# Kernel tuning notes

Measured on AMD Instinct MI355X. Metric: run time of the kernel, lower is better.

Reference implementation:

```python
import jax, jax.numpy as jnp
import numpy as np

N_NODES = 100000
N_EDGES = 1600000
NFEAT = 128
NHID = 128
NCLASS = 40
BN_EPS = 1e-5


def _glorot(key, shape):
    fan_in, fan_out = shape[1], shape[0]
    lim = (6.0 / (fan_in + fan_out)) ** 0.5
    return jax.random.uniform(key, shape, jnp.float32, -lim, lim)


def setup_inputs() -> dict:
    key = jax.random.key(0)
    ks = jax.random.split(key, 16)
    x = jax.random.normal(ks[0], (N_NODES, NFEAT), jnp.float32)
    src = jax.random.randint(ks[1], (N_EDGES,), 0, N_NODES, jnp.int64)
    dst = jax.random.randint(ks[2], (N_EDGES,), 0, N_NODES, jnp.int64)
    edge_index = jnp.stack([src, dst])  # [2, E]
    return {
        "x": x,
        "edge_index": edge_index,
        # conv1: nfeat -> nhid (lin_l with bias on aggregated msgs, lin_r no bias on root)
        "W1l": _glorot(ks[3], (NHID, NFEAT)), "b1": jnp.zeros((NHID,), jnp.float32),
        "W1r": _glorot(ks[4], (NHID, NFEAT)),
        # convx[0]: nhid -> nhid
        "Wxl": _glorot(ks[5], (NHID, NHID)), "bx": jnp.zeros((NHID,), jnp.float32),
        "Wxr": _glorot(ks[6], (NHID, NHID)),
        # conv2: nhid -> nclass
        "W2l": _glorot(ks[7], (NCLASS, NHID)), "b2": jnp.zeros((NCLASS,), jnp.float32),
        "W2r": _glorot(ks[8], (NCLASS, NHID)),
        # batch_norm3 (nhid) and batch_norm2 (nclass)
        "g3": jnp.ones((NHID,), jnp.float32), "be3": jnp.zeros((NHID,), jnp.float32),
        "g2": jnp.ones((NCLASS,), jnp.float32), "be2": jnp.zeros((NCLASS,), jnp.float32),
    }


def _sage_conv(x, src, dst, Wl, b, Wr):
    # mean aggregation of source features at destination nodes
    msg = x[src]                                                  # [E, F] gather
    agg = jax.ops.segment_sum(msg, dst, num_segments=N_NODES)    # [N, F] scatter-add
    cnt = jax.ops.segment_sum(jnp.ones((msg.shape[0],), x.dtype), dst, num_segments=N_NODES)
    mean = agg / jnp.maximum(cnt, 1.0)[:, None]                   # empty neighborhoods -> 0
    return mean @ Wl.T + b + x @ Wr.T


def _batch_norm(x, gamma, beta):
    mu = jnp.mean(x, axis=0)
    var = jnp.mean(jnp.square(x - mu), axis=0)  # biased var (training-mode BN)
    return (x - mu) * jax.lax.rsqrt(var + BN_EPS) * gamma + beta


def reference(x, edge_index, W1l, b1, W1r, Wxl, bx, Wxr, W2l, b2, W2r, g3, be3, g2, be2):
    src, dst = edge_index[0], edge_index[1]
    h = _sage_conv(x, src, dst, W1l, b1, W1r)      # conv1
    h = jax.nn.relu(h)
    # convx loop (nlayer - 2 == 1); dropout p=0 is identity
    h = _sage_conv(h, src, dst, Wxl, bx, Wxr)
    h = _batch_norm(h, g3, be3)                    # batch_norm3 (BN=True)
    h = jax.nn.relu(h)
    h = _sage_conv(h, src, dst, W2l, b2, W2r)      # conv2
    h = _batch_norm(h, g2, be2)                    # batch_norm2
    return h
```

## Files before the change

kernel.cpp:

```cpp
#include <hip/hip_runtime.h>
#include <hip/hip_bf16.h>

#define NN 100000
#define NE 1600000
#define NF 128
#define NC 40
#define BN_EPS 1e-5f

#define NB 256
#define NBU ((NN + 511) >> 9)
#define PT_TILE 4096
#define PT_GRID ((NE + PT_TILE - 1) / PT_TILE)

typedef __attribute__((ext_vector_type(8))) short short8;
typedef __attribute__((ext_vector_type(4))) float float4v;
typedef __attribute__((ext_vector_type(4))) int int4v;

__device__ __forceinline__ unsigned short f2b(float f) {
    __hip_bfloat16 h = __float2bfloat16(f);
    return *reinterpret_cast<unsigned short*>(&h);
}
__device__ __forceinline__ float b2f_hi(unsigned u) { return __uint_as_float(u & 0xffff0000u); }
__device__ __forceinline__ float b2f_lo(unsigned u) { return __uint_as_float(u << 16); }


__global__ __launch_bounds__(256) void bhist_kernel(const int* __restrict__ dst,
                                                    int* __restrict__ bhist) {
    __shared__ int lh[NB];
    int tid = threadIdx.x;
    lh[tid] = 0;
    __syncthreads();
    int base = blockIdx.x * PT_TILE;
    int cnt = min(PT_TILE, NE - base);
    const int4v* d4 = (const int4v*)(dst + base);
    int cnt4 = cnt >> 2;
    for (int i = tid; i < cnt4; i += 256) {
        int4v d = __builtin_nontemporal_load(d4 + i);
        atomicAdd(&lh[d[0] >> 9], 1);
        atomicAdd(&lh[d[1] >> 9], 1);
        atomicAdd(&lh[d[2] >> 9], 1);
        atomicAdd(&lh[d[3] >> 9], 1);
    }
    __syncthreads();
    if (lh[tid]) atomicAdd(&bhist[tid], lh[tid]);
}
// ... 107 lines not shown

__global__ __launch_bounds__(1024) void scan3_kernel(const int* __restrict__ deg,
                                                     const int* __restrict__ row_loc,
                                                     const int* __restrict__ blockoff,
                                                     int* __restrict__ row_ptr,
                                                     float* __restrict__ inv_cnt) {
    int i = blockIdx.x * 1024 + threadIdx.x;
    if (i < NN) {
        row_ptr[i] = blockoff[blockIdx.x] + row_loc[i];
        int d = deg[i];
        inv_cnt[i] = 1.0f / (float)(d > 0 ? d : 1);
    }
    if (i == 0) row_ptr[NN] = NE;
}

__global__ __launch_bounds__(256) void bucket_fill_kernel(const long long* __restrict__ stage,
                                                          const int* __restrict__ bbase,
                                                          const int* __restrict__ bcur,
                                                          const int* __restrict__ row_ptr,
                                                          int* __restrict__ cursor,
                                                          int* __restrict__ csr) {
    int b = blockIdx.x;
    int s = bbase[b], e = bcur[b];
    for (int i = s + threadIdx.x; i < e; i += 256) {
        long long p = __builtin_nontemporal_load(stage + i);
        int d = (int)(p & 0xffffffffLL);
        int sv = (int)(p >> 32);
        int pos = atomicAdd(&cursor[d], 1);
        csr[row_ptr[d] + pos] = sv;
    }
}


__global__ __launch_bounds__(256) void f2b4_kernel(const float* __restrict__ in,
                                                   unsigned short* __restrict__ out, int n4) {
    int i = blockIdx.x * 256 + threadIdx.x;
    if (i < n4) {
        float4 v = ((const float4*)in)[i];
        ushort4 o;
        o.x = f2b(v.x); o.y = f2b(v.y); o.z = f2b(v.z); o.w = f2b(v.w);
        ((ushort4*)out)[i] = o;
    }
}


__global__ __launch_bounds__(64) void pack_w_kernel(const float* __restrict__ Wl,
                                                    const float* __restrict__ Wr,
                                                    unsigned short* __restrict__ Bp) {
    int nt = blockIdx.x & 7;
    int kk = blockIdx.x >> 3;
    int lane = threadIdx.x;
    int n = nt * 16 + (lane & 15);
    int kb = kk * 32 + (lane >> 4) * 8;
    size_t base = ((size_t)(kk * 8 + nt) * 64 + lane) * 8;
#pragma unroll
    for (int j = 0; j < 8; ++j) {
        int k = kb + j;
        float v = (k < NF) ? Wl[(size_t)n * NF + k] : Wr[(size_t)n * NF + (k - NF)];
        Bp[base + j] = f2b(v);
    }
}

__global__ __launch_bounds__(64) void pack_w80_kernel(const float* __restrict__ Wl,
                                                      const float* __restrict__ Wr,
                                                      unsigned short* __restrict__ Bp) {
    int nt = blockIdx.x % 5;
    int kk = blockIdx.x / 5;
    int lane = threadIdx.x;
    int n = nt * 16 + (lane & 15);
    int kb = kk * 32 + (lane >> 4) * 8;
    size_t base = ((size_t)(kk * 5 + nt) * 64 + lane) * 8;
#pragma unroll
    for (int j = 0; j < 8; ++j) {
        int k = kb + j;
        float v = (n < NC) ? Wl[(size_t)n * NF + k] : Wr[(size_t)(n - NC) * NF + k];
        Bp[base + j] = f2b(v);
    }
}


__device__ __forceinline__ void acc8(float* a, uint4 u) {
    a[0] += b2f_lo(u.x); a[1] += b2f_hi(u.x);
    a[2] += b2f_lo(u.y); a[3] += b2f_hi(u.y);
    a[4] += b2f_lo(u.z); a[5] += b2f_hi(u.z);
    a[6] += b2f_lo(u.w); a[7] += b2f_hi(u.w);
}

__global__ __launch_bounds__(256) void agg_mean_bf16(const unsigned short* __restrict__ X,
                                                     const int* __restrict__ csr,
                                                     const int* __restrict__ row_ptr,
                                                     const float* __restrict__ inv_cnt,
                                                     unsigned short* __restrict__ out) {
    int tid = threadIdx.x;
    int lane = tid & 63;
    int wave = tid >> 6;
    int qw = lane >> 4;
    int sl = lane & 15;
    int n = blockIdx.x * 16 + wave * 4 + qw;
    if (n >= NN) return;
    int s = row_ptr[n], e = row_ptr[n + 1];
    int foff = sl * 8;

    float a[8];
#pragma unroll
    for (int j = 0; j < 8; ++j) a[j] = 0.f;

    int i = s;
    for (; i + 4 <= e; i += 4) {
        int s0 = csr[i], s1 = csr[i + 1], s2 = csr[i + 2], s3 = csr[i + 3];
        uint4 u0 = *(const uint4*)(X + (size_t)s0 * NF + foff);
        uint4 u1 = *(const uint4*)(X + (size_t)s1 * NF + foff);
        uint4 u2 = *(const uint4*)(X + (size_t)s2 * NF + foff);
        uint4 u3 = *(const uint4*)(X + (size_t)s3 * NF + foff);
        acc8(a, u0); acc8(a, u1); acc8(a, u2); acc8(a, u3);
    }
    for (; i < e; ++i) {
        uint4 u = *(const uint4*)(X + (size_t)csr[i] * NF + foff);
        acc8(a, u);
    }

    float ic = inv_cnt[n];
    uint4 o;
    o.x = (unsigned)f2b(a[0] * ic) | ((unsigned)f2b(a[1] * ic) << 16);
    o.y = (unsigned)f2b(a[2] * ic) | ((unsigned)f2b(a[3] * ic) << 16);
    o.z = (unsigned)f2b(a[4] * ic) | ((unsigned)f2b(a[5] * ic) << 16);
    o.w = (unsigned)f2b(a[6] * ic) | ((unsigned)f2b(a[7] * ic) << 16);
    *(uint4*)(out + (size_t)n * NF + foff) = o;
}


template <bool RELU>
__global__ __launch_bounds__(256, 5) void lin_mfma_kernel(const unsigned short* __restrict__ Ab,
                                                          const unsigned short* __restrict__ Xb,
                                                          const unsigned short* __restrict__ Bp,
                                                          const float* __restrict__ bias,
                                                          unsigned short* __restrict__ outb) {
    int tid = threadIdx.x;
    int wave = tid >> 6;
    int lane = tid & 63;
    int quad = lane >> 4;
    int row = blockIdx.x * 64 + wave * 16 + (lane & 15);
    int rowc = row < NN ? row : (NN - 1);
    const unsigned short* arow = Ab + (size_t)rowc * NF;
    const unsigned short* xrow = Xb + (size_t)rowc * NF;
    const short8* Bv = (const short8*)Bp;

    float4v acc[8];
#pragma unroll
    for (int nt = 0; nt < 8; ++nt) acc[nt] = (float4v){0.f, 0.f, 0.f, 0.f};

#pragma unroll
    for (int kk = 0; kk < 8; ++kk) {
        int kb = (kk & 3) * 32 + quad * 8;
        const unsigned short* asrc = (kk < 4) ? arow : xrow;
        short8 afrag = *(const short8*)(asrc + kb);
#pragma unroll
        for (int nt = 0; nt < 8; ++nt) {
            short8 bfrag = Bv[(kk * 8 + nt) * 64 + lane];
            acc[nt] = __builtin_amdgcn_mfma_f32_16x16x32_bf16(afrag, bfrag, acc[nt], 0, 0, 0);
        }
    }

    int orow = blockIdx.x * 64 + wave * 16 + quad * 4;
    int col = lane & 15;
#pragma unroll
    for (int nt = 0; nt < 8; ++nt) {
        int c = nt * 16 + col;
        float bv = bias[c];
#pragma unroll
        for (int r = 0; r < 4; ++r) {
            int rr = orow + r;
            if (rr < NN) {
                float v = acc[nt][r] + bv;
                if (RELU) v = fmaxf(v, 0.f);
                outb[(size_t)rr * NF + c] = f2b(v);
            }
        }
    }
}


__global__ __launch_bounds__(256, 5) void lin80_mfma_kernel(const unsigned short* __restrict__ Xb,
                                                            const unsigned short* __restrict__ Bp,
                                                            const float* __restrict__ b2,
                                                            unsigned short* __restrict__ t40,
                                                            float* __restrict__ z40) {
    int tid = threadIdx.x;
    int wave = tid >> 6;
    int lane = tid & 63;
    int quad = lane >> 4;
    int row = blockIdx.x * 64 + wave * 16 + (lane & 15);
    int rowc = row < NN ? row : (NN - 1);
    const unsigned short* xrow = Xb + (size_t)rowc * NF;
    const short8* Bv = (const short8*)Bp;

    float4v acc[5];
#pragma unroll
    for (int nt = 0; nt < 5; ++nt) acc[nt] = (float4v){0.f, 0.f, 0.f, 0.f};

#pragma unroll
    for (int kk = 0; kk < 4; ++kk) {
        int kb = kk * 32 + quad * 8;
        short8 afrag = *(const short8*)(xrow + kb);
#pragma unroll
        for (int nt = 0; nt < 5; ++nt) {
            short8 bfrag = Bv[(kk * 5 + nt) * 64 + lane];
            acc[nt] = __builtin_amdgcn_mfma_f32_16x16x32_bf16(afrag, bfrag, acc[nt], 0, 0, 0);
        }
    }

    int orow = blockIdx.x * 64 + wave * 16 + quad * 4;
    int col = lane & 15;
#pragma unroll
    for (int nt = 0; nt < 5; ++nt) {
        int c = nt * 16 + col;
#pragma unroll
        for (int r = 0; r < 4; ++r) {
            int rr = orow + r;
            if (rr < NN) {
                float v = acc[nt][r];
                if (c < NC) {
                    t40[(size_t)rr * NC + c] = f2b(v);
                } else {
                    z40[(size_t)rr * NC + (c - NC)] = v + b2[c - NC];
                }
            }
        }
    }
}


__global__ __launch_bounds__(256) void agg40_add_bf16(const unsigned short* __restrict__ T,
                                                      const float* __restrict__ Z,
                                                      const int* __restrict__ csr,
                                                      const int* __restrict__ row_ptr,
                                                      const float* __restrict__ inv_cnt,
                                                      float* __restrict__ out) {
    int tid = threadIdx.x;
    int lane = tid & 63;
    int wave = tid >> 6;
    if (lane >= 60) return;
    int sub = lane / 20;
    int sl = lane % 20;
    int n = blockIdx.x * 12 + wave * 3 + sub;
    if (n >= NN) return;
    int s = row_ptr[n], e = row_ptr[n + 1];
    float a0 = 0.f, a1 = 0.f;
    int i = s;
    for (; i + 4 <= e; i += 4) {
        int s0 = csr[i], s1 = csr[i + 1], s2 = csr[i + 2], s3 = csr[i + 3];
        unsigned u0 = *(const unsigned*)(T + (size_t)s0 * NC + sl * 2);
        unsigned u1 = *(const unsigned*)(T + (size_t)s1 * NC + sl * 2);
        unsigned u2 = *(const unsigned*)(T + (size_t)s2 * NC + sl * 2);
        unsigned u3 = *(const unsigned*)(T + (size_t)s3 * NC + sl * 2);
        a0 += b2f_lo(u0) + b2f_lo(u1) + b2f_lo(u2) + b2f_lo(u3);
        a1 += b2f_hi(u0) + b2f_hi(u1) + b2f_hi(u2) + b2f_hi(u3);
    }
    for (; i < e; ++i) {
        unsigned u = *(const unsigned*)(T + (size_t)csr[i] * NC + sl * 2);
        a0 += b2f_lo(u);
        a1 += b2f_hi(u);
    }
    float ic = inv_cnt[n];
    const float2 zv = *(const float2*)(Z + (size_t)n * NC + sl * 2);
    float2 o;
    o.x = a0 * ic + zv.x;
    o.y = a1 * ic + zv.y;
    *(float2*)(out + (size_t)n * NC + sl * 2) = o;
}

#define BN_GRID 640

template <int F>
__global__ __launch_bounds__(256) void bn_stats2_kernel(const float* __restrict__ X,
                                                        float* __restrict__ sums) {
    __shared__ float ls[2 * F];
    int tid = threadIdx.x;
    for (int i = tid; i < 2 * F; i += 256) ls[i] = 0.f;
    __syncthreads();

    const int total4 = NN * F / 4;
    const int stride = BN_GRID * 256;
    int i0 = blockIdx.x * 256 + tid;
    int c0 = (i0 * 4) % F;
    float s0 = 0.f, s1 = 0.f, s2 = 0.f, s3 = 0.f;
    float q0 = 0.f, q1 = 0.f, q2 = 0.f, q3 = 0.f;
    for (int i = i0; i < total4; i += stride) {
        float4 v = ((const float4*)X)[i];
        s0 += v.x; q0 += v.x * v.x;
        s1 += v.y; q1 += v.y * v.y;
        s2 += v.z; q2 += v.z * v.z;
        s3 += v.w; q3 += v.w * v.w;
    }
    atomicAdd(&ls[c0 + 0], s0); atomicAdd(&ls[F + c0 + 0], q0);
    atomicAdd(&ls[c0 + 1], s1); atomicAdd(&ls[F + c0 + 1], q1);
    atomicAdd(&ls[c0 + 2], s2); atomicAdd(&ls[F + c0 + 2], q2);
    atomicAdd(&ls[c0 + 3], s3); atomicAdd(&ls[F + c0 + 3], q3);
    __syncthreads();
    for (int i = tid; i < 2 * F; i += 256) atomicAdd(&sums[i], ls[i]);
}

__global__ __launch_bounds__(256) void bn_stats_b16_kernel(const unsigned short* __restrict__ H,
                                                           float* __restrict__ sums) {
    __shared__ float ls[2 * NF];
    int tid = threadIdx.x;
    for (int i = tid; i < 2 * NF; i += 256) ls[i] = 0.f;
    __syncthreads();

    const int total8 = NN * NF / 8;
    const int stride = BN_GRID * 256;
    int i0 = blockIdx.x * 256 + tid;
    int c0 = (i0 * 8) & (NF - 1);
    float s[8], q[8];
#pragma unroll
    for (int j = 0; j < 8; ++j) { s[j] = 0.f; q[j] = 0.f; }
    for (int i = i0; i < total8; i += stride) {
        uint4 u = ((const uint4*)H)[i];
        float v;
        v = b2f_lo(u.x); s[0] += v; q[0] += v * v;
        v = b2f_hi(u.x); s[1] += v; q[1] += v * v;
        v = b2f_lo(u.y); s[2] += v; q[2] += v * v;
        v = b2f_hi(u.y); s[3] += v; q[3] += v * v;
        v = b2f_lo(u.z); s[4] += v; q[4] += v * v;
        v = b2f_hi(u.z); s[5] += v; q[5] += v * v;
        v = b2f_lo(u.w); s[6] += v; q[6] += v * v;
        v = b2f_hi(u.w); s[7] += v; q[7] += v * v;
    }
#pragma unroll
    for (int j = 0; j < 8; ++j) {
        atomicAdd(&ls[c0 + j], s[j]);
        atomicAdd(&ls[NF + c0 + j], q[j]);
    }
    __syncthreads();
    for (int i = tid; i < 2 * NF; i += 256) atomicAdd(&sums[i], ls[i]);
}

__global__ __launch_bounds__(256) void bn3_apply_b16_kernel(unsigned* __restrict__ H,
                                                            const float* __restrict__ sums,
                                                            const float* __restrict__ g,
                                                            const float* __restrict__ be,
                                                            float invN) {
    int idx = blockIdx.x * 256 + threadIdx.x;
    if (idx >= NN * NF / 2) return;
    int t0 = (idx * 2) & (NF - 1);
    float mu0 = sums[t0] * invN, mu1 = sums[t0 + 1] * invN;
    float var0 = sums[NF + t0] * invN - mu0 * mu0;
    float var1 = sums[NF + t0 + 1] * invN - mu1 * mu1;
    float sc0 = rsqrtf(var0 + BN_EPS) * g[t0];
    float sc1 = rsqrtf(var1 + BN_EPS) * g[t0 + 1];
    unsigned u = H[idx];
    float v0 = fmaxf((b2f_lo(u) - mu0) * sc0 + be[t0], 0.f);
    float v1 = fmaxf((b2f_hi(u) - mu1) * sc1 + be[t0 + 1], 0.f);
    H[idx] = (unsigned)f2b(v0) | ((unsigned)f2b(v1) << 16);
}

template <bool RELU>
__global__ __launch_bounds__(256) void bn_apply_kernel(float* __restrict__ X,
                                                       const float* __restrict__ sums,
                                                       const float* __restrict__ g,
                                                       const float* __restrict__ be,
                                                       int F, float invN) {
    size_t idx = (size_t)blockIdx.x * blockDim.x + threadIdx.x;
    size_t total = (size_t)NN * F;
    if (idx >= total) return;
    int t = (int)(idx % F);
    float mu = sums[t] * invN;
    float var = sums[F + t] * invN - mu * mu;
    float scale = rsqrtf(var + BN_EPS) * g[t];
    float v = (X[idx] - mu) * scale + be[t];
    if (RELU) v = fmaxf(v, 0.f);
    X[idx] = v;
}


extern "C" void kernel_launch(void* const* d_in, const int* in_sizes, int n_in,
                              void* d_out, int out_size, void* d_ws, size_t ws_size,
                              hipStream_t stream) {
    const float* x   = (const float*)d_in[0];
    const int*   ei  = (const int*)d_in[1];
    const int*   srcv = ei;
    const int*   dstv = ei + NE;
    const float* W1l = (const float*)d_in[2];
    const float* b1  = (const float*)d_in[3];
    const float* W1r = (const float*)d_in[4];
    const float* Wxl = (const float*)d_in[5];
    const float* bx  = (const float*)d_in[6];
    const float* Wxr = (const float*)d_in[7];
    const float* W2l = (const float*)d_in[8];
    const float* b2  = (const float*)d_in[9];
    const float* W2r = (const float*)d_in[10];
    const float* g3  = (const float*)d_in[11];
    const float* be3 = (const float*)d_in[12];
    const float* g2  = (const float*)d_in[13];
    const float* be2 = (const float*)d_in[14];
    float* out = (float*)d_out;

    char* w = (char*)d_ws;
    unsigned short* xb   = (unsigned short*)w; w += (size_t)NN * NF * 2;
    unsigned short* h1b  = (unsigned short*)w; w += (size_t)NN * NF * 2;
    unsigned short* aggb = (unsigned short*)w; w += (size_t)NN * NF * 2;
    unsigned short* h2b  = (unsigned short*)w; w += (size_t)NN * NF * 2;
    int* csr     = (int*)w; w += (size_t)NE * 4;
    int* row_ptr = (int*)w; w += (size_t)(NN + 4) * 4;
    int* deg     = (int*)w; w += (size_t)NN * 4;
    int* cursor  = (int*)w; w += (size_t)NN * 4;
    int* row_loc = (int*)w; w += (size_t)NN * 4;
    int* blocksum = (int*)w; w += 128 * 4;
    float* inv_cnt = (float*)w; w += (size_t)NN * 4;
    float* bnbuf3  = (float*)w; w += 2 * NF * 4;
    float* bnbuf2  = (float*)w; w += 2 * NC * 4;
    unsigned short* Bp1 = (unsigned short*)w; w += (size_t)256 * NF * 2;
    unsigned short* Bpx = (unsigned short*)w; w += (size_t)256 * NF * 2;
    unsigned short* Bp2 = (unsigned short*)w; w += (size_t)128 * 80 * 2;
    int* bhist = (int*)w; w += NB * 4;
    int* bbase = (int*)w; w += NB * 4;
    int* bcurA = (int*)w; w += NB * 4;
    int2* stage = (int2*)h2b;
    unsigned short* t40 = xb;
    float* z40 = (float*)h1b;

    const int nscan = (NN + 1023) / 1024;

    hipMemsetAsync(deg, 0, (size_t)NN * 4, stream);
    hipMemsetAsync(cursor, 0, (size_t)NN * 4, stream);
    hipMemsetAsync(bhist, 0, NB * 4, stream);
    hipMemsetAsync(bnbuf3, 0, 2 * NF * 4, stream);
    hipMemsetAsync(bnbuf2, 0, 2 * NC * 4, stream);

    bhist_kernel<<<PT_GRID, 256, 0, stream>>>(dstv, bhist);
    bscan_kernel<<<1, 256, 0, stream>>>(bhist, bbase, bcurA);
    part_kernel<<<PT_GRID, 256, 0, stream>>>(srcv, dstv, bcurA, stage);
    bucket_deg_kernel<<<NBU, 256, 0, stream>>>((const long long*)stage, bbase, bcurA, deg);
    scan1_kernel<<<nscan, 1024, 0, stream>>>(deg, row_loc, blocksum);
    scan2_kernel<<<1, 128, 0, stream>>>(blocksum, nscan);
    scan3_kernel<<<nscan, 1024, 0, stream>>>(deg, row_loc, blocksum, row_ptr, inv_cnt);
    bucket_fill_kernel<<<NBU, 256, 0, stream>>>((const long long*)stage, bbase, bcurA,
                                                row_ptr, cursor, csr);

    f2b4_kernel<<<(NN * NF / 4 + 255) / 256, 256, 0, stream>>>(x, xb, NN * NF / 4);
    pack_w_kernel<<<64, 64, 0, stream>>>(W1l, W1r, Bp1);
    pack_w_kernel<<<64, 64, 0, stream>>>(Wxl, Wxr, Bpx);
    pack_w80_kernel<<<20, 64, 0, stream>>>(W2l, W2r, Bp2);

    const int nblk_lin = (NN + 63) / 64;
    const int nblk_agg = (NN + 15) / 16;

    agg_mean_bf16<<<nblk_agg, 256, 0, stream>>>(xb, csr, row_ptr, inv_cnt, aggb);
    lin_mfma_kernel<true><<<nblk_lin, 256, 0, stream>>>(aggb, xb, Bp1, b1, h1b);

    agg_mean_bf16<<<nblk_agg, 256, 0, stream>>>(h1b, csr, row_ptr, inv_cnt, aggb);
    lin_mfma_kernel<false><<<nblk_lin, 256, 0, stream>>>(aggb, h1b, Bpx, bx, h2b);

    bn_stats_b16_kernel<<<BN_GRID, 256, 0, stream>>>(h2b, bnbuf3);
    bn3_apply_b16_kernel<<<(NN * NF / 2 + 255) / 256, 256, 0, stream>>>((unsigned*)h2b, bnbuf3, g3, be3, 1.0f / NN);

    lin80_mfma_kernel<<<nblk_lin, 256, 0, stream>>>(h2b, Bp2, b2, t40, z40);
    agg40_add_bf16<<<(NN + 11) / 12, 256, 0, stream>>>(t40, z40, csr, row_ptr, inv_cnt, out);

    bn_stats2_kernel<NC><<<BN_GRID, 256, 0, stream>>>(out, bnbuf2);
    bn_apply_kernel<false><<<(NN * NC + 255) / 256, 256, 0, stream>>>(out, bnbuf2, g2, be2, NC, 1.0f / NN);
}
```

Baseline: 583.2 us.

## Fuse BN3 stats into linear epilogue, BN apply into lin80, degree-sort aggregation

Batch-norm statistics for the hidden layer are now accumulated in the MFMA linear kernel's epilogue, and the normalize+ReLU is applied on the fly when lin80 loads its A fragments. This removes a separate stats pass and an in-place apply pass over the 100k×128 bf16 tensor. Aggregation kernels now process nodes in degree-bucketed order via a counting-sort permutation and unroll the gather by 8, aiming to balance per-wave work and raise memory-level parallelism. The cost is three small extra preprocessing kernels plus shared/global atomics in the linear epilogue, and BN stats are now taken from fp32 values before bf16 rounding.

```diff
diff --git a/kernel.cpp b/kernel.cpp
--- a/kernel.cpp
+++ b/kernel.cpp
@@ -184,6 +184,66 @@
 }
 
 
+__global__ __launch_bounds__(256) void dhist_kernel(const int* __restrict__ deg,
+                                                    int* __restrict__ dh) {
+    __shared__ int lh[64];
+    int tid = threadIdx.x;
+    if (tid < 64) lh[tid] = 0;
+    __syncthreads();
+    int i0 = blockIdx.x * 1024 + tid;
+#pragma unroll
+    for (int j = 0; j < 4; ++j) {
+        int i = i0 + j * 256;
+        if (i < NN) atomicAdd(&lh[min(deg[i], 63)], 1);
+    }
+    __syncthreads();
+    if (tid < 64 && lh[tid]) atomicAdd(&dh[tid], lh[tid]);
+}
+
+__global__ __launch_bounds__(64) void dscan_kernel(const int* __restrict__ dh,
+                                                   int* __restrict__ dcur) {
+    int t = threadIdx.x;
+    int v = dh[t];
+    int x = v;
+    for (int off = 1; off < 64; off <<= 1) {
+        int u = __shfl_up(x, off);
+        if (t >= off) x += u;
+    }
+    dcur[t] = x - v;
+}
+
+__global__ __launch_bounds__(256) void dscatter_kernel(const int* __restrict__ deg,
+                                                       int* __restrict__ dcur,
+                                                       int* __restrict__ perm) {
+    __shared__ int lh[64], lb[64];
+    int tid = threadIdx.x;
+    if (tid < 64) lh[tid] = 0;
+    __syncthreads();
+    int i0 = blockIdx.x * 1024 + tid;
+#pragma unroll
+    for (int j = 0; j < 4; ++j) {
+        int i = i0 + j * 256;
+        if (i < NN) atomicAdd(&lh[min(deg[i], 63)], 1);
+    }
+    __syncthreads();
+    if (tid < 64) {
+        int c = lh[tid];
+        lb[tid] = (c > 0) ? atomicAdd(&dcur[tid], c) : 0;
+        lh[tid] = 0;
+    }
+    __syncthreads();
+#pragma unroll
+    for (int j = 0; j < 4; ++j) {
+        int i = i0 + j * 256;
+        if (i < NN) {
+            int b = min(deg[i], 63);
+            int p = atomicAdd(&lh[b], 1);
+            perm[lb[b] + p] = i;
+        }
+    }
+}
+
+
 __global__ __launch_bounds__(256) void f2b4_kernel(const float* __restrict__ in,
                                                    unsigned short* __restrict__ out, int n4) {
     int i = blockIdx.x * 256 + threadIdx.x;
@@ -242,32 +302,49 @@
                                                      const int* __restrict__ csr,
                                                      const int* __restrict__ row_ptr,
                                                      const float* __restrict__ inv_cnt,
+                                                     const int* __restrict__ perm,
                                                      unsigned short* __restrict__ out) {
     int tid = threadIdx.x;
     int lane = tid & 63;
     int wave = tid >> 6;
     int qw = lane >> 4;
     int sl = lane & 15;
-    int n = blockIdx.x * 16 + wave * 4 + qw;
-    if (n >= NN) return;
+    int g = blockIdx.x * 16 + wave * 4 + qw;
+    if (g >= NN) return;
+    int n = perm[g];
     int s = row_ptr[n], e = row_ptr[n + 1];
-    int foff = sl * 8;
+    const unsigned short* Xf = X + sl * 8;
 
     float a[8];
 #pragma unroll
     for (int j = 0; j < 8; ++j) a[j] = 0.f;
 
     int i = s;
-    for (; i + 4 <= e; i += 4) {
+    for (; i + 8 <= e; i += 8) {
         int s0 = csr[i], s1 = csr[i + 1], s2 = csr[i + 2], s3 = csr[i + 3];
-        uint4 u0 = *(const uint4*)(X + (size_t)s0 * NF + foff);
-        uint4 u1 = *(const uint4*)(X + (size_t)s1 * NF + foff);
-        uint4 u2 = *(const uint4*)(X + (size_t)s2 * NF + foff);
-        uint4 u3 = *(const uint4*)(X + (size_t)s3 * NF + foff);
+        int s4 = csr[i + 4], s5 = csr[i + 5], s6 = csr[i + 6], s7 = csr[i + 7];
+        uint4 u0 = *(const uint4*)(Xf + (size_t)s0 * NF);
+        uint4 u1 = *(const uint4*)(Xf + (size_t)s1 * NF);
+        uint4 u2 = *(const uint4*)(Xf + (size_t)s2 * NF);
+        uint4 u3 = *(const uint4*)(Xf + (size_t)s3 * NF);
+        uint4 u4 = *(const uint4*)(Xf + (size_t)s4 * NF);
+        uint4 u5 = *(const uint4*)(Xf + (size_t)s5 * NF);
+        uint4 u6 = *(const uint4*)(Xf + (size_t)s6 * NF);
+        uint4 u7 = *(const uint4*)(Xf + (size_t)s7 * NF);
         acc8(a, u0); acc8(a, u1); acc8(a, u2); acc8(a, u3);
+        acc8(a, u4); acc8(a, u5); acc8(a, u6); acc8(a, u7);
+    }
+    if (i + 4 <= e) {
+        int s0 = csr[i], s1 = csr[i + 1], s2 = csr[i + 2], s3 = csr[i + 3];
+        uint4 u0 = *(const uint4*)(Xf + (size_t)s0 * NF);
+        uint4 u1 = *(const uint4*)(Xf + (size_t)s1 * NF);
+        uint4 u2 = *(const uint4*)(Xf + (size_t)s2 * NF);
+        uint4 u3 = *(const uint4*)(Xf + (size_t)s3 * NF);
+        acc8(a, u0); acc8(a, u1); acc8(a, u2); acc8(a, u3);
+        i += 4;
     }
     for (; i < e; ++i) {
-        uint4 u = *(const uint4*)(X + (size_t)csr[i] * NF + foff);
+        uint4 u = *(const uint4*)(Xf + (size_t)csr[i] * NF);
         acc8(a, u);
     }
 
@@ -277,16 +354,18 @@
     o.y = (unsigned)f2b(a[2] * ic) | ((unsigned)f2b(a[3] * ic) << 16);
     o.z = (unsigned)f2b(a[4] * ic) | ((unsigned)f2b(a[5] * ic) << 16);
     o.w = (unsigned)f2b(a[6] * ic) | ((unsigned)f2b(a[7] * ic) << 16);
-    *(uint4*)(out + (size_t)n * NF + foff) = o;
-}
-
-
-template <bool RELU>
+    *(uint4*)(out + (size_t)n * NF + sl * 8) = o;
+}
+
+
+template <bool RELU, bool STATS>
 __global__ __launch_bounds__(256, 5) void lin_mfma_kernel(const unsigned short* __restrict__ Ab,
                                                           const unsigned short* __restrict__ Xb,
                                                           const unsigned short* __restrict__ Bp,
                                                           const float* __restrict__ bias,
-                                                          unsigned short* __restrict__ outb) {
+                                                          unsigned short* __restrict__ outb,
+                                                          float* __restrict__ sums) {
+    __shared__ float ls[256];
     int tid = threadIdx.x;
     int wave = tid >> 6;
     int lane = tid & 63;
@@ -297,6 +376,11 @@
     const unsigned short* xrow = Xb + (size_t)rowc * NF;
     const short8* Bv = (const short8*)Bp;
 
+    if (STATS) {
+        ls[tid] = 0.f;
+        __syncthreads();
+    }
+
     float4v acc[8];
 #pragma unroll
     for (int nt = 0; nt < 8; ++nt) acc[nt] = (float4v){0.f, 0.f, 0.f, 0.f};
@@ -319,22 +403,49 @@
     for (int nt = 0; nt < 8; ++nt) {
         int c = nt * 16 + col;
         float bv = bias[c];
+        float sv = 0.f, qv = 0.f;
 #pragma unroll
         for (int r = 0; r < 4; ++r) {
             int rr = orow + r;
             if (rr < NN) {
                 float v = acc[nt][r] + bv;
                 if (RELU) v = fmaxf(v, 0.f);
+                if (STATS) { sv += v; qv += v * v; }
                 outb[(size_t)rr * NF + c] = f2b(v);
             }
         }
-    }
+        if (STATS) {
+            atomicAdd(&ls[c], sv);
+            atomicAdd(&ls[128 + c], qv);
+        }
+    }
+    if (STATS) {
+        __syncthreads();
+        atomicAdd(&sums[tid], ls[tid]);
+    }
+}
+
+
+__global__ __launch_bounds__(128) void bn3_coef_kernel(const float* __restrict__ sums,
+                                                       const float* __restrict__ g,
+                                                       const float* __restrict__ be,
+                                                       float* __restrict__ sc,
+                                                       float* __restrict__ sh) {
+    int c = threadIdx.x;
+    float invN = 1.0f / (float)NN;
+    float mu = sums[c] * invN;
+    float var = sums[NF + c] * invN - mu * mu;
+    float s = rsqrtf(var + BN_EPS) * g[c];
+    sc[c] = s;
+    sh[c] = be[c] - mu * s;
 }
 
 
 __global__ __launch_bounds__(256, 5) void lin80_mfma_kernel(const unsigned short* __restrict__ Xb,
                                                             const unsigned short* __restrict__ Bp,
                                                             const float* __restrict__ b2,
+                                                            const float* __restrict__ bnsc,
+                                                            const float* __restrict__ bnsh,
                                                             unsigned short* __restrict__ t40,
                                                             float* __restrict__ z40) {
     int tid = threadIdx.x;
@@ -353,7 +464,20 @@
 #pragma unroll
     for (int kk = 0; kk < 4; ++kk) {
         int kb = kk * 32 + quad * 8;
-        short8 afrag = *(const short8*)(xrow + kb);
+        uint4 u = *(const uint4*)(xrow + kb);
+        float4 c0 = *(const float4*)(bnsc + kb);
+        float4 c1 = *(const float4*)(bnsc + kb + 4);
+        float4 h0 = *(const float4*)(bnsh + kb);
+        float4 h1 = *(const float4*)(bnsh + kb + 4);
+        short8 afrag;
+        afrag[0] = (short)f2b(fmaxf(b2f_lo(u.x) * c0.x + h0.x, 0.f));
+        afrag[1] = (short)f2b(fmaxf(b2f_hi(u.x) * c0.y + h0.y, 0.f));
+        afrag[2] = (short)f2b(fmaxf(b2f_lo(u.y) * c0.z + h0.z, 0.f));
+        afrag[3] = (short)f2b(fmaxf(b2f_hi(u.y) * c0.w + h0.w, 0.f));
+        afrag[4] = (short)f2b(fmaxf(b2f_lo(u.z) * c1.x + h1.x, 0.f));
+        afrag[5] = (short)f2b(fmaxf(b2f_hi(u.z) * c1.y + h1.y, 0.f));
+        afrag[6] = (short)f2b(fmaxf(b2f_lo(u.w) * c1.z + h1.z, 0.f));
+        afrag[7] = (short)f2b(fmaxf(b2f_hi(u.w) * c1.w + h1.w, 0.f));
 #pragma unroll
         for (int nt = 0; nt < 5; ++nt) {
             short8 bfrag = Bv[(kk * 5 + nt) * 64 + lane];
@@ -387,6 +511,7 @@
                                                       const int* __restrict__ csr,
                                                       const int* __restrict__ row_ptr,
                                                       const float* __restrict__ inv_cnt,
+                                                      const int* __restrict__ perm,
                                                       float* __restrict__ out) {
     int tid = threadIdx.x;
     int lane = tid & 63;
@@ -394,22 +519,41 @@
     if (lane >= 60) return;
     int sub = lane / 20;
     int sl = lane % 20;
-    int n = blockIdx.x * 12 + wave * 3 + sub;
-    if (n >= NN) return;
+    int g = blockIdx.x * 12 + wave * 3 + sub;
+    if (g >= NN) return;
+    int n = perm[g];
     int s = row_ptr[n], e = row_ptr[n + 1];
+    const unsigned short* Tf = T + sl * 2;
     float a0 = 0.f, a1 = 0.f;
     int i = s;
-    for (; i + 4 <= e; i += 4) {
+    for (; i + 8 <= e; i += 8) {
         int s0 = csr[i], s1 = csr[i + 1], s2 = csr[i + 2], s3 = csr[i + 3];
-        unsigned u0 = *(const unsigned*)(T + (size_t)s0 * NC + sl * 2);
-        unsigned u1 = *(const unsigned*)(T + (size_t)s1 * NC + sl * 2);
-        unsigned u2 = *(const unsigned*)(T + (size_t)s2 * NC + sl * 2);
-        unsigned u3 = *(const unsigned*)(T + (size_t)s3 * NC + sl * 2);
+        int s4 = csr[i + 4], s5 = csr[i + 5], s6 = csr[i + 6], s7 = csr[i + 7];
+        unsigned u0 = *(const unsigned*)(Tf + (size_t)s0 * NC);
+        unsigned u1 = *(const unsigned*)(Tf + (size_t)s1 * NC);
+        unsigned u2 = *(const unsigned*)(Tf + (size_t)s2 * NC);
+        unsigned u3 = *(const unsigned*)(Tf + (size_t)s3 * NC);
+        unsigned u4 = *(const unsigned*)(Tf + (size_t)s4 * NC);
+        unsigned u5 = *(const unsigned*)(Tf + (size_t)s5 * NC);
+        unsigned u6 = *(const unsigned*)(Tf + (size_t)s6 * NC);
+        unsigned u7 = *(const unsigned*)(Tf + (size_t)s7 * NC);
+        a0 += b2f_lo(u0) + b2f_lo(u1) + b2f_lo(u2) + b2f_lo(u3)
+            + b2f_lo(u4) + b2f_lo(u5) + b2f_lo(u6) + b2f_lo(u7);
+        a1 += b2f_hi(u0) + b2f_hi(u1) + b2f_hi(u2) + b2f_hi(u3)
+            + b2f_hi(u4) + b2f_hi(u5) + b2f_hi(u6) + b2f_hi(u7);
+    }
+    if (i + 4 <= e) {
+        int s0 = csr[i], s1 = csr[i + 1], s2 = csr[i + 2], s3 = csr[i + 3];
+        unsigned u0 = *(const unsigned*)(Tf + (size_t)s0 * NC);
+        unsigned u1 = *(const unsigned*)(Tf + (size_t)s1 * NC);
+        unsigned u2 = *(const unsigned*)(Tf + (size_t)s2 * NC);
+        unsigned u3 = *(const unsigned*)(Tf + (size_t)s3 * NC);
         a0 += b2f_lo(u0) + b2f_lo(u1) + b2f_lo(u2) + b2f_lo(u3);
         a1 += b2f_hi(u0) + b2f_hi(u1) + b2f_hi(u2) + b2f_hi(u3);
+        i += 4;
     }
     for (; i < e; ++i) {
-        unsigned u = *(const unsigned*)(T + (size_t)csr[i] * NC + sl * 2);
+        unsigned u = *(const unsigned*)(Tf + (size_t)csr[i] * NC);
         a0 += b2f_lo(u);
         a1 += b2f_hi(u);
     }
@@ -450,60 +594,6 @@
     atomicAdd(&ls[c0 + 3], s3); atomicAdd(&ls[F + c0 + 3], q3);
     __syncthreads();
     for (int i = tid; i < 2 * F; i += 256) atomicAdd(&sums[i], ls[i]);
-}
-
-__global__ __launch_bounds__(256) void bn_stats_b16_kernel(const unsigned short* __restrict__ H,
-                                                           float* __restrict__ sums) {
-    __shared__ float ls[2 * NF];
-    int tid = threadIdx.x;
-    for (int i = tid; i < 2 * NF; i += 256) ls[i] = 0.f;
-    __syncthreads();
-
-    const int total8 = NN * NF / 8;
-    const int stride = BN_GRID * 256;
-    int i0 = blockIdx.x * 256 + tid;
-    int c0 = (i0 * 8) & (NF - 1);
-    float s[8], q[8];
-#pragma unroll
-    for (int j = 0; j < 8; ++j) { s[j] = 0.f; q[j] = 0.f; }
-    for (int i = i0; i < total8; i += stride) {
-        uint4 u = ((const uint4*)H)[i];
-        float v;
-        v = b2f_lo(u.x); s[0] += v; q[0] += v * v;
-        v = b2f_hi(u.x); s[1] += v; q[1] += v * v;
-        v = b2f_lo(u.y); s[2] += v; q[2] += v * v;
-        v = b2f_hi(u.y); s[3] += v; q[3] += v * v;
-        v = b2f_lo(u.z); s[4] += v; q[4] += v * v;
-        v = b2f_hi(u.z); s[5] += v; q[5] += v * v;
-        v = b2f_lo(u.w); s[6] += v; q[6] += v * v;
-        v = b2f_hi(u.w); s[7] += v; q[7] += v * v;
-    }
-#pragma unroll
-    for (int j = 0; j < 8; ++j) {
-        atomicAdd(&ls[c0 + j], s[j]);
-        atomicAdd(&ls[NF + c0 + j], q[j]);
-    }
-    __syncthreads();
-    for (int i = tid; i < 2 * NF; i += 256) atomicAdd(&sums[i], ls[i]);
-}
-
-__global__ __launch_bounds__(256) void bn3_apply_b16_kernel(unsigned* __restrict__ H,
-                                                            const float* __restrict__ sums,
-                                                            const float* __restrict__ g,
-                                                            const float* __restrict__ be,
-                                                            float invN) {
-    int idx = blockIdx.x * 256 + threadIdx.x;
-    if (idx >= NN * NF / 2) return;
-    int t0 = (idx * 2) & (NF - 1);
-    float mu0 = sums[t0] * invN, mu1 = sums[t0 + 1] * invN;
-    float var0 = sums[NF + t0] * invN - mu0 * mu0;
-    float var1 = sums[NF + t0 + 1] * invN - mu1 * mu1;
-    float sc0 = rsqrtf(var0 + BN_EPS) * g[t0];
-    float sc1 = rsqrtf(var1 + BN_EPS) * g[t0 + 1];
-    unsigned u = H[idx];
-    float v0 = fmaxf((b2f_lo(u) - mu0) * sc0 + be[t0], 0.f);
-    float v1 = fmaxf((b2f_hi(u) - mu1) * sc1 + be[t0 + 1], 0.f);
-    H[idx] = (unsigned)f2b(v0) | ((unsigned)f2b(v1) << 16);
 }
 
 template <bool RELU>
@@ -561,12 +651,17 @@
     float* inv_cnt = (float*)w; w += (size_t)NN * 4;
     float* bnbuf3  = (float*)w; w += 2 * NF * 4;
     float* bnbuf2  = (float*)w; w += 2 * NC * 4;
+    float* bnsc    = (float*)w; w += NF * 4;
+    float* bnsh    = (float*)w; w += NF * 4;
     unsigned short* Bp1 = (unsigned short*)w; w += (size_t)256 * NF * 2;
     unsigned short* Bpx = (unsigned short*)w; w += (size_t)256 * NF * 2;
     unsigned short* Bp2 = (unsigned short*)w; w += (size_t)128 * 80 * 2;
     int* bhist = (int*)w; w += NB * 4;
     int* bbase = (int*)w; w += NB * 4;
     int* bcurA = (int*)w; w += NB * 4;
+    int* dh    = (int*)w; w += 64 * 4;
+    int* dcur  = (int*)w; w += 64 * 4;
+    int* perm  = (int*)w; w += (size_t)NN * 4;
     int2* stage = (int2*)h2b;
     unsigned short* t40 = xb;
     float* z40 = (float*)h1b;
@@ -576,6 +671,7 @@
     hipMemsetAsync(deg, 0, (size_t)NN * 4, stream);
     hipMemsetAsync(cursor, 0, (size_t)NN * 4, stream);
     hipMemsetAsync(bhist, 0, NB * 4, stream);
+    hipMemsetAsync(dh, 0, 64 * 4, stream);
     hipMemsetAsync(bnbuf3, 0, 2 * NF * 4, stream);
     hipMemsetAsync(bnbuf2, 0, 2 * NC * 4, stream);
 
@@ -583,6 +679,9 @@
     bscan_kernel<<<1, 256, 0, stream>>>(bhist, bbase, bcurA);
     part_kernel<<<PT_GRID, 256, 0, stream>>>(srcv, dstv, bcurA, stage);
     bucket_deg_kernel<<<NBU, 256, 0, stream>>>((const long long*)stage, bbase, bcurA, deg);
+    dhist_kernel<<<nscan, 256, 0, stream>>>(deg, dh);
+    dscan_kernel<<<1, 64, 0, stream>>>(dh, dcur);
+    dscatter_kernel<<<nscan, 256, 0, stream>>>(deg, dcur, perm);
     scan1_kernel<<<nscan, 1024, 0, stream>>>(deg, row_loc, blocksum);
     scan2_kernel<<<1, 128, 0, stream>>>(blocksum, nscan);
     scan3_kernel<<<nscan, 1024, 0, stream>>>(deg, row_loc, blocksum, row_ptr, inv_cnt);
@@ -597,17 +696,16 @@
     const int nblk_lin = (NN + 63) / 64;
     const int nblk_agg = (NN + 15) / 16;
 
-    agg_mean_bf16<<<nblk_agg, 256, 0, stream>>>(xb, csr, row_ptr, inv_cnt, aggb);
-    lin_mfma_kernel<true><<<nblk_lin, 256, 0, stream>>>(aggb, xb, Bp1, b1, h1b);
-
-    agg_mean_bf16<<<nblk_agg, 256, 0, stream>>>(h1b, csr, row_ptr, inv_cnt, aggb);
-    lin_mfma_kernel<false><<<nblk_lin, 256, 0, stream>>>(aggb, h1b, Bpx, bx, h2b);
-
-    bn_stats_b16_kernel<<<BN_GRID, 256, 0, stream>>>(h2b, bnbuf3);
-    bn3_apply_b16_kernel<<<(NN * NF / 2 + 255) / 256, 256, 0, stream>>>((unsigned*)h2b, bnbuf3, g3, be3, 1.0f / NN);
-
-    lin80_mfma_kernel<<<nblk_lin, 256, 0, stream>>>(h2b, Bp2, b2, t40, z40);
-    agg40_add_bf16<<<(NN + 11) / 12, 256, 0, stream>>>(t40, z40, csr, row_ptr, inv_cnt, out);
+    agg_mean_bf16<<<nblk_agg, 256, 0, stream>>>(xb, csr, row_ptr, inv_cnt, perm, aggb);
+    lin_mfma_kernel<true, false><<<nblk_lin, 256, 0, stream>>>(aggb, xb, Bp1, b1, h1b, nullptr);
+
+    agg_mean_bf16<<<nblk_agg, 256, 0, stream>>>(h1b, csr, row_ptr, inv_cnt, perm, aggb);
+    lin_mfma_kernel<false, true><<<nblk_lin, 256, 0, stream>>>(aggb, h1b, Bpx, bx, h2b, bnbuf3);
+
+    bn3_coef_kernel<<<1, 128, 0, stream>>>(bnbuf3, g3, be3, bnsc, bnsh);
+
+    lin80_mfma_kernel<<<nblk_lin, 256, 0, stream>>>(h2b, Bp2, b2, bnsc, bnsh, t40, z40);
+    agg40_add_bf16<<<(NN + 11) / 12, 256, 0, stream>>>(t40, z40, csr, row_ptr, inv_cnt, perm, out);
 
     bn_stats2_kernel<NC><<<BN_GRID, 256, 0, stream>>>(out, bnbuf2);
     bn_apply_kernel<false><<<(NN * NC + 255) / 256, 256, 0, stream>>>(out, bnbuf2, g2, be2, NC, 1.0f / NN);
```

Measured after the change: 601.2 us. +3.1%, slower.

## Fuse BN3 stats into convx GEMM and BN3 apply into conv2 GEMM

Applied to the files above, without the earlier changes.

The linear kernels become persistent grid-stride loops that keep the packed weight fragments in registers and swap MFMA operands, so each wave owns column slices and writes vectorised outputs. The convx GEMM accumulates per-column sum and sum-of-squares into banked atomics, and a tiny kernel turns them into scale/shift. The conv2 GEMM then applies BN and ReLU on the fly when loading its input, which removes the separate stats pass and the read-modify-write apply pass over h2. In exchange, BN statistics are now computed from fp32 values before bf16 rounding, and more registers are held per thread.

```diff
diff --git a/kernel.cpp b/kernel.cpp
--- a/kernel.cpp
+++ b/kernel.cpp
@@ -11,6 +11,10 @@
 #define NBU ((NN + 511) >> 9)
 #define PT_TILE 4096
 #define PT_GRID ((NE + PT_TILE - 1) / PT_TILE)
+#define SBANK 32
+#define NTILES (NN / 16)
+#define LIN_GRID 1250
+#define LIN80_GRID 512
 
 typedef __attribute__((ext_vector_type(8))) short short8;
 typedef __attribute__((ext_vector_type(4))) float float4v;
@@ -281,101 +285,217 @@
 }
 
 
-template <bool RELU>
-__global__ __launch_bounds__(256, 5) void lin_mfma_kernel(const unsigned short* __restrict__ Ab,
-                                                          const unsigned short* __restrict__ Xb,
-                                                          const unsigned short* __restrict__ Bp,
-                                                          const float* __restrict__ bias,
-                                                          unsigned short* __restrict__ outb) {
+template <bool RELU, bool STATS>
+__device__ __forceinline__ void lin_body(const unsigned short* __restrict__ Ab,
+                                         const unsigned short* __restrict__ Xb,
+                                         const unsigned short* __restrict__ Bp,
+                                         const float* __restrict__ bias,
+                                         unsigned short* __restrict__ outb,
+                                         float* __restrict__ sums,
+                                         float* ls) {
     int tid = threadIdx.x;
     int wave = tid >> 6;
     int lane = tid & 63;
     int quad = lane >> 4;
-    int row = blockIdx.x * 64 + wave * 16 + (lane & 15);
-    int rowc = row < NN ? row : (NN - 1);
-    const unsigned short* arow = Ab + (size_t)rowc * NF;
-    const unsigned short* xrow = Xb + (size_t)rowc * NF;
+    int sl = lane & 15;
     const short8* Bv = (const short8*)Bp;
 
-    float4v acc[8];
-#pragma unroll
-    for (int nt = 0; nt < 8; ++nt) acc[nt] = (float4v){0.f, 0.f, 0.f, 0.f};
-
-#pragma unroll
-    for (int kk = 0; kk < 8; ++kk) {
-        int kb = (kk & 3) * 32 + quad * 8;
-        const unsigned short* asrc = (kk < 4) ? arow : xrow;
-        short8 afrag = *(const short8*)(asrc + kb);
-#pragma unroll
-        for (int nt = 0; nt < 8; ++nt) {
-            short8 bfrag = Bv[(kk * 8 + nt) * 64 + lane];
-            acc[nt] = __builtin_amdgcn_mfma_f32_16x16x32_bf16(afrag, bfrag, acc[nt], 0, 0, 0);
+    if (STATS) {
+        ls[tid] = 0.f;
+        __syncthreads();
+    }
+
+    short8 bfr[8][2];
+#pragma unroll
+    for (int kk = 0; kk < 8; ++kk)
+#pragma unroll
+        for (int j = 0; j < 2; ++j)
+            bfr[kk][j] = Bv[(kk * 8 + 2 * wave + j) * 64 + lane];
+
+    float4 bias4[2];
+#pragma unroll
+    for (int j = 0; j < 2; ++j)
+        bias4[j] = *(const float4*)(bias + (2 * wave + j) * 16 + quad * 4);
+
+    float sts[2][4], stq[2][4];
+    if (STATS) {
+#pragma unroll
+        for (int j = 0; j < 2; ++j)
+#pragma unroll
+            for (int r = 0; r < 4; ++r) { sts[j][r] = 0.f; stq[j][r] = 0.f; }
+    }
+
+    for (int t = blockIdx.x; t < NTILES; t += LIN_GRID) {
+        int rr = t * 16 + sl;
+        const unsigned short* arow = Ab + (size_t)rr * NF;
+        const unsigned short* xrow = Xb + (size_t)rr * NF;
+
+        short8 xf[8];
+#pragma unroll
+        for (int kk = 0; kk < 8; ++kk) {
+            int kb = (kk & 3) * 32 + quad * 8;
+            const unsigned short* asrc = (kk < 4) ? arow : xrow;
+            xf[kk] = *(const short8*)(asrc + kb);
         }
-    }
-
-    int orow = blockIdx.x * 64 + wave * 16 + quad * 4;
-    int col = lane & 15;
-#pragma unroll
-    for (int nt = 0; nt < 8; ++nt) {
-        int c = nt * 16 + col;
-        float bv = bias[c];
-#pragma unroll
-        for (int r = 0; r < 4; ++r) {
-            int rr = orow + r;
-            if (rr < NN) {
-                float v = acc[nt][r] + bv;
-                if (RELU) v = fmaxf(v, 0.f);
-                outb[(size_t)rr * NF + c] = f2b(v);
+
+        float4v acc[2];
+#pragma unroll
+        for (int j = 0; j < 2; ++j) acc[j] = (float4v){0.f, 0.f, 0.f, 0.f};
+
+#pragma unroll
+        for (int kk = 0; kk < 8; ++kk)
+#pragma unroll
+            for (int j = 0; j < 2; ++j)
+                acc[j] = __builtin_amdgcn_mfma_f32_16x16x32_bf16(bfr[kk][j], xf[kk], acc[j], 0, 0, 0);
+
+#pragma unroll
+        for (int j = 0; j < 2; ++j) {
+            int c0 = (2 * wave + j) * 16 + quad * 4;
+            float v0 = acc[j][0] + bias4[j].x;
+            float v1 = acc[j][1] + bias4[j].y;
+            float v2 = acc[j][2] + bias4[j].z;
+            float v3 = acc[j][3] + bias4[j].w;
+            if (RELU) {
+                v0 = fmaxf(v0, 0.f); v1 = fmaxf(v1, 0.f);
+                v2 = fmaxf(v2, 0.f); v3 = fmaxf(v3, 0.f);
+            }
+            if (STATS) {
+                sts[j][0] += v0; stq[j][0] += v0 * v0;
+                sts[j][1] += v1; stq[j][1] += v1 * v1;
+                sts[j][2] += v2; stq[j][2] += v2 * v2;
+                sts[j][3] += v3; stq[j][3] += v3 * v3;
+            }
+            ushort4 o;
+            o.x = f2b(v0); o.y = f2b(v1); o.z = f2b(v2); o.w = f2b(v3);
+            *(ushort4*)(outb + (size_t)rr * NF + c0) = o;
+        }
+    }
+
+    if (STATS) {
+#pragma unroll
+        for (int j = 0; j < 2; ++j) {
+            int c0 = (2 * wave + j) * 16 + quad * 4;
+#pragma unroll
+            for (int r = 0; r < 4; ++r) {
+                atomicAdd(&ls[c0 + r], sts[j][r]);
+                atomicAdd(&ls[128 + c0 + r], stq[j][r]);
             }
         }
-    }
-}
-
-
-__global__ __launch_bounds__(256, 5) void lin80_mfma_kernel(const unsigned short* __restrict__ Xb,
+        __syncthreads();
+        atomicAdd(&sums[(blockIdx.x & (SBANK - 1)) * 256 + tid], ls[tid]);
+    }
+}
+
+__global__ __launch_bounds__(256, 3) void lin_conv1_kernel(const unsigned short* __restrict__ Ab,
+                                                           const unsigned short* __restrict__ Xb,
+                                                           const unsigned short* __restrict__ Bp,
+                                                           const float* __restrict__ bias,
+                                                           unsigned short* __restrict__ outb) {
+    lin_body<true, false>(Ab, Xb, Bp, bias, outb, nullptr, nullptr);
+}
+
+__global__ __launch_bounds__(256, 3) void lin_convx_kernel(const unsigned short* __restrict__ Ab,
+                                                           const unsigned short* __restrict__ Xb,
+                                                           const unsigned short* __restrict__ Bp,
+                                                           const float* __restrict__ bias,
+                                                           unsigned short* __restrict__ outb,
+                                                           float* __restrict__ sums) {
+    __shared__ float ls[256];
+    lin_body<false, true>(Ab, Xb, Bp, bias, outb, sums, ls);
+}
+
+
+__global__ __launch_bounds__(128) void bn3_coef_kernel(const float* __restrict__ sums,
+                                                       const float* __restrict__ g,
+                                                       const float* __restrict__ be,
+                                                       float* __restrict__ sc,
+                                                       float* __restrict__ sh) {
+    int c = threadIdx.x;
+    float sv = 0.f, qv = 0.f;
+    for (int b = 0; b < SBANK; ++b) {
+        sv += sums[b * 256 + c];
+        qv += sums[b * 256 + 128 + c];
+    }
+    float invN = 1.0f / (float)NN;
+    float mu = sv * invN;
+    float var = qv * invN - mu * mu;
+    float s = rsqrtf(var + BN_EPS) * g[c];
+    sc[c] = s;
+    sh[c] = be[c] - mu * s;
+}
+
+
+__global__ __launch_bounds__(256, 2) void lin80_mfma_kernel(const unsigned short* __restrict__ Xb,
                                                             const unsigned short* __restrict__ Bp,
                                                             const float* __restrict__ b2,
+                                                            const float* __restrict__ bnsc,
+                                                            const float* __restrict__ bnsh,
                                                             unsigned short* __restrict__ t40,
                                                             float* __restrict__ z40) {
     int tid = threadIdx.x;
     int wave = tid >> 6;
     int lane = tid & 63;
     int quad = lane >> 4;
-    int row = blockIdx.x * 64 + wave * 16 + (lane & 15);
-    int rowc = row < NN ? row : (NN - 1);
-    const unsigned short* xrow = Xb + (size_t)rowc * NF;
+    int sl = lane & 15;
     const short8* Bv = (const short8*)Bp;
 
-    float4v acc[5];
-#pragma unroll
-    for (int nt = 0; nt < 5; ++nt) acc[nt] = (float4v){0.f, 0.f, 0.f, 0.f};
-
+    short8 bfr[4][5];
+#pragma unroll
+    for (int kk = 0; kk < 4; ++kk)
+#pragma unroll
+        for (int nt = 0; nt < 5; ++nt)
+            bfr[kk][nt] = Bv[(kk * 5 + nt) * 64 + lane];
+
+    float4 sc0[4], sc1[4], sh0[4], sh1[4];
 #pragma unroll
     for (int kk = 0; kk < 4; ++kk) {
         int kb = kk * 32 + quad * 8;
-        short8 afrag = *(const short8*)(xrow + kb);
+        sc0[kk] = *(const float4*)(bnsc + kb);
+        sc1[kk] = *(const float4*)(bnsc + kb + 4);
+        sh0[kk] = *(const float4*)(bnsh + kb);
+        sh1[kk] = *(const float4*)(bnsh + kb + 4);
+    }
+
+    int gw = blockIdx.x * 4 + wave;
+    for (int t = gw; t < NTILES; t += LIN80_GRID * 4) {
+        int rr = t * 16 + sl;
+        const unsigned short* xrow = Xb + (size_t)rr * NF;
+
+        float4v acc[5];
+#pragma unroll
+        for (int nt = 0; nt < 5; ++nt) acc[nt] = (float4v){0.f, 0.f, 0.f, 0.f};
+
+#pragma unroll
+        for (int kk = 0; kk < 4; ++kk) {
+            uint4 u = *(const uint4*)(xrow + kk * 32 + quad * 8);
+            short8 xf;
+            xf[0] = (short)f2b(fmaxf(b2f_lo(u.x) * sc0[kk].x + sh0[kk].x, 0.f));
+            xf[1] = (short)f2b(fmaxf(b2f_hi(u.x) * sc0[kk].y + sh0[kk].y, 0.f));
+            xf[2] = (short)f2b(fmaxf(b2f_lo(u.y) * sc0[kk].z + sh0[kk].z, 0.f));
+            xf[3] = (short)f2b(fmaxf(b2f_hi(u.y) * sc0[kk].w + sh0[kk].w, 0.f));
+            xf[4] = (short)f2b(fmaxf(b2f_lo(u.z) * sc1[kk].x + sh1[kk].x, 0.f));
+            xf[5] = (short)f2b(fmaxf(b2f_hi(u.z) * sc1[kk].y + sh1[kk].y, 0.f));
+            xf[6] = (short)f2b(fmaxf(b2f_lo(u.w) * sc1[kk].z + sh1[kk].z, 0.f));
+            xf[7] = (short)f2b(fmaxf(b2f_hi(u.w) * sc1[kk].w + sh1[kk].w, 0.f));
+#pragma unroll
+            for (int nt = 0; nt < 5; ++nt)
+                acc[nt] = __builtin_amdgcn_mfma_f32_16x16x32_bf16(bfr[kk][nt], xf, acc[nt], 0, 0, 0);
+        }
+
 #pragma unroll
         for (int nt = 0; nt < 5; ++nt) {
-            short8 bfrag = Bv[(kk * 5 + nt) * 64 + lane];
-            acc[nt] = __builtin_amdgcn_mfma_f32_16x16x32_bf16(afrag, bfrag, acc[nt], 0, 0, 0);
-        }
-    }
-
-    int orow = blockIdx.x * 64 + wave * 16 + quad * 4;
-    int col = lane & 15;
-#pragma unroll
-    for (int nt = 0; nt < 5; ++nt) {
-        int c = nt * 16 + col;
-#pragma unroll
-        for (int r = 0; r < 4; ++r) {
-            int rr = orow + r;
-            if (rr < NN) {
-                float v = acc[nt][r];
-                if (c < NC) {
-                    t40[(size_t)rr * NC + c] = f2b(v);
-                } else {
-                    z40[(size_t)rr * NC + (c - NC)] = v + b2[c - NC];
-                }
+            int c0 = nt * 16 + quad * 4;
+            if (c0 < NC) {
+                ushort4 o;
+                o.x = f2b(acc[nt][0]); o.y = f2b(acc[nt][1]);
+                o.z = f2b(acc[nt][2]); o.w = f2b(acc[nt][3]);
+                *(ushort4*)(t40 + (size_t)rr * NC + c0) = o;
+            } else {
+                float4 bz = *(const float4*)(b2 + c0 - NC);
+                float4 o;
+                o.x = acc[nt][0] + bz.x; o.y = acc[nt][1] + bz.y;
+                o.z = acc[nt][2] + bz.z; o.w = acc[nt][3] + bz.w;
+                *(float4*)(z40 + (size_t)rr * NC + (c0 - NC)) = o;
             }
         }
     }
@@ -397,19 +517,20 @@
     int n = blockIdx.x * 12 + wave * 3 + sub;
     if (n >= NN) return;
     int s = row_ptr[n], e = row_ptr[n + 1];
+    const unsigned short* Tf = T + sl * 2;
     float a0 = 0.f, a1 = 0.f;
     int i = s;
     for (; i + 4 <= e; i += 4) {
         int s0 = csr[i], s1 = csr[i + 1], s2 = csr[i + 2], s3 = csr[i + 3];
-        unsigned u0 = *(const unsigned*)(T + (size_t)s0 * NC + sl * 2);
-        unsigned u1 = *(const unsigned*)(T + (size_t)s1 * NC + sl * 2);
-        unsigned u2 = *(const unsigned*)(T + (size_t)s2 * NC + sl * 2);
-        unsigned u3 = *(const unsigned*)(T + (size_t)s3 * NC + sl * 2);
+        unsigned u0 = *(const unsigned*)(Tf + (size_t)s0 * NC);
+        unsigned u1 = *(const unsigned*)(Tf + (size_t)s1 * NC);
+        unsigned u2 = *(const unsigned*)(Tf + (size_t)s2 * NC);
+        unsigned u3 = *(const unsigned*)(Tf + (size_t)s3 * NC);
         a0 += b2f_lo(u0) + b2f_lo(u1) + b2f_lo(u2) + b2f_lo(u3);
         a1 += b2f_hi(u0) + b2f_hi(u1) + b2f_hi(u2) + b2f_hi(u3);
     }
     for (; i < e; ++i) {
-        unsigned u = *(const unsigned*)(T + (size_t)csr[i] * NC + sl * 2);
+        unsigned u = *(const unsigned*)(Tf + (size_t)csr[i] * NC);
         a0 += b2f_lo(u);
         a1 += b2f_hi(u);
     }
@@ -450,60 +571,6 @@
     atomicAdd(&ls[c0 + 3], s3); atomicAdd(&ls[F + c0 + 3], q3);
     __syncthreads();
     for (int i = tid; i < 2 * F; i += 256) atomicAdd(&sums[i], ls[i]);
-}
-
-__global__ __launch_bounds__(256) void bn_stats_b16_kernel(const unsigned short* __restrict__ H,
-                                                           float* __restrict__ sums) {
-    __shared__ float ls[2 * NF];
-    int tid = threadIdx.x;
-    for (int i = tid; i < 2 * NF; i += 256) ls[i] = 0.f;
-    __syncthreads();
-
-    const int total8 = NN * NF / 8;
-    const int stride = BN_GRID * 256;
-    int i0 = blockIdx.x * 256 + tid;
-    int c0 = (i0 * 8) & (NF - 1);
-    float s[8], q[8];
-#pragma unroll
-    for (int j = 0; j < 8; ++j) { s[j] = 0.f; q[j] = 0.f; }
-    for (int i = i0; i < total8; i += stride) {
-        uint4 u = ((const uint4*)H)[i];
-        float v;
-        v = b2f_lo(u.x); s[0] += v; q[0] += v * v;
-        v = b2f_hi(u.x); s[1] += v; q[1] += v * v;
-        v = b2f_lo(u.y); s[2] += v; q[2] += v * v;
-        v = b2f_hi(u.y); s[3] += v; q[3] += v * v;
-        v = b2f_lo(u.z); s[4] += v; q[4] += v * v;
-        v = b2f_hi(u.z); s[5] += v; q[5] += v * v;
-        v = b2f_lo(u.w); s[6] += v; q[6] += v * v;
-        v = b2f_hi(u.w); s[7] += v; q[7] += v * v;
-    }
-#pragma unroll
-    for (int j = 0; j < 8; ++j) {
-        atomicAdd(&ls[c0 + j], s[j]);
-        atomicAdd(&ls[NF + c0 + j], q[j]);
-    }
-    __syncthreads();
-    for (int i = tid; i < 2 * NF; i += 256) atomicAdd(&sums[i], ls[i]);
-}
-
-__global__ __launch_bounds__(256) void bn3_apply_b16_kernel(unsigned* __restrict__ H,
-                                                            const float* __restrict__ sums,
-                                                            const float* __restrict__ g,
-                                                            const float* __restrict__ be,
-                                                            float invN) {
-    int idx = blockIdx.x * 256 + threadIdx.x;
-    if (idx >= NN * NF / 2) return;
-    int t0 = (idx * 2) & (NF - 1);
-    float mu0 = sums[t0] * invN, mu1 = sums[t0 + 1] * invN;
-    float var0 = sums[NF + t0] * invN - mu0 * mu0;
-    float var1 = sums[NF + t0 + 1] * invN - mu1 * mu1;
-    float sc0 = rsqrtf(var0 + BN_EPS) * g[t0];
-    float sc1 = rsqrtf(var1 + BN_EPS) * g[t0 + 1];
-    unsigned u = H[idx];
-    float v0 = fmaxf((b2f_lo(u) - mu0) * sc0 + be[t0], 0.f);
-    float v1 = fmaxf((b2f_hi(u) - mu1) * sc1 + be[t0 + 1], 0.f);
-    H[idx] = (unsigned)f2b(v0) | ((unsigned)f2b(v1) << 16);
 }
 
 template <bool RELU>
@@ -559,8 +626,10 @@
     int* row_loc = (int*)w; w += (size_t)NN * 4;
     int* blocksum = (int*)w; w += 128 * 4;
     float* inv_cnt = (float*)w; w += (size_t)NN * 4;
-    float* bnbuf3  = (float*)w; w += 2 * NF * 4;
+    float* bnbuf3  = (float*)w; w += (size_t)SBANK * 256 * 4;
     float* bnbuf2  = (float*)w; w += 2 * NC * 4;
+    float* bnsc    = (float*)w; w += NF * 4;
+    float* bnsh    = (float*)w; w += NF * 4;
     unsigned short* Bp1 = (unsigned short*)w; w += (size_t)256 * NF * 2;
     unsigned short* Bpx = (unsigned short*)w; w += (size_t)256 * NF * 2;
     unsigned short* Bp2 = (unsigned short*)w; w += (size_t)128 * 80 * 2;
@@ -576,7 +645,7 @@
     hipMemsetAsync(deg, 0, (size_t)NN * 4, stream);
     hipMemsetAsync(cursor, 0, (size_t)NN * 4, stream);
     hipMemsetAsync(bhist, 0, NB * 4, stream);
-    hipMemsetAsync(bnbuf3, 0, 2 * NF * 4, stream);
+    hipMemsetAsync(bnbuf3, 0, (size_t)SBANK * 256 * 4, stream);
     hipMemsetAsync(bnbuf2, 0, 2 * NC * 4, stream);
 
     bhist_kernel<<<PT_GRID, 256, 0, stream>>>(dstv, bhist);
@@ -594,19 +663,17 @@
     pack_w_kernel<<<64, 64, 0, stream>>>(Wxl, Wxr, Bpx);
     pack_w80_kernel<<<20, 64, 0, stream>>>(W2l, W2r, Bp2);
 
-    const int nblk_lin = (NN + 63) / 64;
     const int nblk_agg = (NN + 15) / 16;
 
     agg_mean_bf16<<<nblk_agg, 256, 0, stream>>>(xb, csr, row_ptr, inv_cnt, aggb);
-    lin_mfma_kernel<true><<<nblk_lin, 256, 0, stream>>>(aggb, xb, Bp1, b1, h1b);
+    lin_conv1_kernel<<<LIN_GRID, 256, 0, stream>>>(aggb, xb, Bp1, b1, h1b);
 
     agg_mean_bf16<<<nblk_agg, 256, 0, stream>>>(h1b, csr, row_ptr, inv_cnt, aggb);
-    lin_mfma_kernel<false><<<nblk_lin, 256, 0, stream>>>(aggb, h1b, Bpx, bx, h2b);
-
-    bn_stats_b16_kernel<<<BN_GRID, 256, 0, stream>>>(h2b, bnbuf3);
-    bn3_apply_b16_kernel<<<(NN * NF / 2 + 255) / 256, 256, 0, stream>>>((unsigned*)h2b, bnbuf3, g3, be3, 1.0f / NN);
-
-    lin80_mfma_kernel<<<nblk_lin, 256, 0, stream>>>(h2b, Bp2, b2, t40, z40);
+    lin_convx_kernel<<<LIN_GRID, 256, 0, stream>>>(aggb, h1b, Bpx, bx, h2b, bnbuf3);
+
+    bn3_coef_kernel<<<1, 128, 0, stream>>>(bnbuf3, g3, be3, bnsc, bnsh);
+
+    lin80_mfma_kernel<<<LIN80_GRID, 256, 0, stream>>>(h2b, Bp2, b2, bnsc, bnsh, t40, z40);
     agg40_add_bf16<<<(NN + 11) / 12, 256, 0, stream>>>(t40, z40, csr, row_ptr, inv_cnt, out);
 
     bn_stats2_kernel<NC><<<BN_GRID, 256, 0, stream>>>(out, bnbuf2);
```

After: 557.9 us. 4.3% less time.
